# Performance work log

Hardware: AMD Instinct MI355X
Metric: run time of the kernel (lower is better)

Reference implementation:

```python
import jax, jax.numpy as jnp
import numpy as np

ALPHA = 1.702
LIMIT = 7.0


def setup_inputs() -> dict:
    key = jax.random.key(0)
    ks = jax.random.split(key, 7)
    B, S, H, D, E, TOPK = 2, 2048, 2048, 2048, 8, 4
    T = B * S
    hidden_states = jax.random.normal(ks[0], (B, S, H), dtype=jnp.float32)
    gate_up_proj = jax.random.normal(ks[1], (E, H, 2 * D), dtype=jnp.float32) * 0.02
    gate_up_proj_bias = jax.random.normal(ks[2], (E, 2 * D), dtype=jnp.float32) * 0.02
    down_proj = jax.random.normal(ks[3], (E, D, H), dtype=jnp.float32) * 0.02
    down_proj_bias = jax.random.normal(ks[4], (E, H), dtype=jnp.float32) * 0.02
    rw = jax.random.uniform(ks[5], (T, E), dtype=jnp.float32)
    routing_weights = rw / jnp.sum(rw, axis=-1, keepdims=True)
    router_indices = jax.random.randint(ks[6], (T, TOPK), 0, E, dtype=jnp.int64)
    return {
        "hidden_states": hidden_states,
        "gate_up_proj": gate_up_proj,
        "gate_up_proj_bias": gate_up_proj_bias,
        "down_proj": down_proj,
        "down_proj_bias": down_proj_bias,
        "routing_weights": routing_weights,
        "router_indices": router_indices,
    }


def geglu(gate_up):
    # interleaved layout: gate = [..., 0::2], up = [..., 1::2]
    gate = gate_up[..., 0::2]
    up = gate_up[..., 1::2]
    gate = jnp.minimum(gate, LIMIT)
    up = jnp.clip(up, -LIMIT, LIMIT)
    glu = gate * jax.nn.sigmoid(gate * ALPHA)
    return (up + 1.0) * glu


def reference(hidden_states, gate_up_proj, gate_up_proj_bias, down_proj,
              down_proj_bias, routing_weights, router_indices):
    B, S, H = hidden_states.shape
    x = hidden_states.reshape(-1, H)  # [T, H]
    # per-expert batched GEMM: [E, T, 2D]
    gate_up = jnp.einsum('th,ehd->etd', x, gate_up_proj) + gate_up_proj_bias[:, None, :]
    act = geglu(gate_up)  # [E, T, D]
    out = jnp.einsum('etd,edh->eth', act, down_proj) + down_proj_bias[:, None, :]
    # weight by router probs and sum over experts
    out = out * routing_weights.T[:, :, None]  # [E, T, H]
    out = jnp.sum(out, axis=0)
    return out.reshape(B, S, H)
```

## Files before the change

### kernel.cpp

```cpp
#include <hip/hip_runtime.h>
#include <hip/hip_bf16.h>

#define ALPHA 1.702f
#define GLIMIT 7.0f

typedef __attribute__((ext_vector_type(4))) float f32x4;
typedef __attribute__((ext_vector_type(8))) __bf16 bf16x8;
typedef __attribute__((ext_vector_type(8))) short short8;

typedef __attribute__((address_space(3))) unsigned int as3_uint;
typedef const __attribute__((address_space(1))) unsigned int as1_uint;

__device__ __forceinline__ void async_copy16(void* lds, const void* g) {
    __builtin_amdgcn_global_load_lds((as1_uint*)g, (as3_uint*)lds, 16, 0, 0);
}

__device__ __forceinline__ short f2bf(float f) {
    unsigned u = __float_as_uint(f);
    unsigned r = (u + 0x7fffu + ((u >> 16) & 1u)) >> 16;
    return (short)r;
}

__global__ void cvt_bf16_kernel(const float* __restrict__ src,
                                short* __restrict__ dst, int n4) {
    int i = blockIdx.x * blockDim.x + threadIdx.x;
    if (i < n4) {
        float4 v = reinterpret_cast<const float4*>(src)[i];
        short4 o;
        o.x = f2bf(v.x); o.y = f2bf(v.y); o.z = f2bf(v.z); o.w = f2bf(v.w);
        reinterpret_cast<short4*>(dst)[i] = o;
    }
}

__global__ void transpose_cvt(const float* __restrict__ src,
                              short* __restrict__ dst, int R, int C) {
    __shared__ float t[64][65];
    const int z  = blockIdx.z;
    const int c0 = blockIdx.x * 64;
    const int r0 = blockIdx.y * 64;
    const float* s = src + (size_t)z * R * C;
    short* d = dst + (size_t)z * R * C;
    const int tid = threadIdx.x;
#pragma unroll
    for (int i = 0; i < 16; ++i) {
        int idx = i * 256 + tid;
        int r = idx >> 6, c = idx & 63;
        t[r][c] = s[(size_t)(r0 + r) * C + c0 + c];
    }
    __syncthreads();
#pragma unroll
    for (int i = 0; i < 16; ++i) {
        int idx = i * 256 + tid;
        int r = idx >> 6, c = idx & 63;
        d[(size_t)(c0 + r) * R + r0 + c] = f2bf(t[c][r]);
    }
}


struct Gemm1PSrc {
    const short* A; const short* B;
    __device__ __forceinline__ const short* operator()(int t, int h) const {
        int e = t >> 5;
        size_t ko = (size_t)(t & 31) << 6;
        if (h & 2) return B + ((size_t)e << 23) + ((size_t)(h & 1) << 18) + ko;
        return A + ((size_t)(h & 1) << 18) + ko;
    }
};

struct Gemm2Src {
    const short* act; const short* wdt; size_t aoff, boff; int kh;
    __device__ __forceinline__ const short* operator()(int t, int h) const {
        int g = (kh << 7) + t;
        int e = g >> 5;
        size_t ko = (size_t)(g & 31) << 6;
        if (h & 2) return wdt + ((size_t)e << 22) + boff + ((size_t)(h & 1) << 18) + ko;
        return act + ((size_t)e << 23) + aoff + ((size_t)(h & 1) << 18) + ko;
    }
};

#define PH_BAR()  __builtin_amdgcn_s_barrier()
#define PH_LGKM() do { asm volatile("s_waitcnt lgkmcnt(0)" ::: "memory"); \
                       __builtin_amdgcn_sched_barrier(0); } while (0)
#define VMW(n)    asm volatile("s_waitcnt vmcnt(" #n ")" ::: "memory")

template <int NT, int SEG, typename Src, typename Epi>
__device__ __forceinline__ void gemm_8phase(const Src& src, char* smem,
                                            f32x4 (&acc)[8][4], const Epi& epi) {
    const int tid  = threadIdx.x;
    const int lane = tid & 63;
    const int wid  = tid >> 6;
    const int wr   = wid >> 2;
    const int wcol = wid & 3;
    const int lhi  = lane >> 4;
    const int llo  = lane & 15;

    auto stage = [&](int buf, int h, const short* g) {
        char* dst = smem + buf * 65536 + h * 16384;
        {
            int c = tid, r = c >> 3, s = (c & 7) ^ (r & 7);
            async_copy16(dst + c * 16, g + (size_t)r * 2048 + s * 8);
        }
        {
            int c = tid + 512, r = c >> 3, s = (c & 7) ^ (r & 7);
            async_copy16(dst + c * 16, g + (size_t)r * 2048 + s * 8);
        }
    };
    auto ldfrag = [&](int buf, int h, int row, int slot) {
        return *(const bf16x8*)(smem + buf * 65536 + h * 16384 + row * 128 +
                                ((slot ^ (row & 7)) << 4));
    };

    stage(0, 0, src(0, 0)); stage(0, 2, src(0, 2));
    stage(0, 3, src(0, 3)); stage(0, 1, src(0, 1));
    stage(1, 0, src(1, 0)); stage(1, 2, src(1, 2)); stage(1, 3, src(1, 3));
    VMW(8);
    PH_BAR();

    bf16x8 a[4][2], b[4][2];
#pragma unroll
    for (int n = 0; n < 2; ++n) {
        int row = wcol * 32 + n * 16 + llo;
        b[n][0] = ldfrag(0, 2, row, lhi);
        b[n][1] = ldfrag(0, 2, row, 4 + lhi);
    }

    for (int t = 0; t < NT; ++t) {
        const int cur = t & 1, nxt = cur ^ 1;
#pragma unroll
        for (int m = 0; m < 4; ++m) {
            int row = wr * 64 + m * 16 + llo;
            a[m][0] = ldfrag(cur, 0, row, lhi);
            a[m][1] = ldfrag(cur, 0, row, 4 + lhi);
        }
        if (t + 1 < NT) stage(nxt, 1, src(t + 1, 1));
        PH_BAR(); PH_LGKM();
        __builtin_amdgcn_s_setprio(1);
#pragma unroll
        for (int m = 0; m < 4; ++m)
#pragma unroll
            for (int n = 0; n < 2; ++n)
#pragma unroll
                for (int ks = 0; ks < 2; ++ks)
                    acc[m][n] = __builtin_amdgcn_mfma_f32_16x16x32_bf16(
                        a[m][ks], b[n][ks], acc[m][n], 0, 0, 0);
        __builtin_amdgcn_s_setprio(0);
        PH_BAR();
#pragma unroll
        for (int n = 0; n < 2; ++n) {
            int row = wcol * 32 + n * 16 + llo;
            b[2 + n][0] = ldfrag(cur, 3, row, lhi);
            b[2 + n][1] = ldfrag(cur, 3, row, 4 + lhi);
        }
        if (t + 2 < NT) { stage(cur, 0, src(t + 2, 0)); VMW(10); }
        else if (t + 1 < NT) { VMW(8); }
        else { VMW(0); }
        PH_BAR(); PH_LGKM();
        __builtin_amdgcn_s_setprio(1);
#pragma unroll
        for (int m = 0; m < 4; ++m)
#pragma unroll
            for (int n = 2; n < 4; ++n)
#pragma unroll
                for (int ks = 0; ks < 2; ++ks)
                    acc[m][n] = __builtin_amdgcn_mfma_f32_16x16x32_bf16(
                        a[m][ks], b[n][ks], acc[m][n], 0, 0, 0);
        __builtin_amdgcn_s_setprio(0);
        PH_BAR();
#pragma unroll
        for (int m = 0; m < 4; ++m) {
            int row = wr * 64 + m * 16 + llo;
            a[m][0] = ldfrag(cur, 1, row, lhi);
            a[m][1] = ldfrag(cur, 1, row, 4 + lhi);
        }
        if (t + 2 < NT) stage(cur, 2, src(t + 2, 2));
        PH_BAR(); PH_LGKM();
        __builtin_amdgcn_s_setprio(1);
#pragma unroll
        for (int m = 0; m < 4; ++m)
#pragma unroll
            for (int n = 0; n < 2; ++n)
#pragma unroll
                for (int ks = 0; ks < 2; ++ks)
                    acc[4 + m][n] = __builtin_amdgcn_mfma_f32_16x16x32_bf16(
                        a[m][ks], b[n][ks], acc[4 + m][n], 0, 0, 0);
        __builtin_amdgcn_s_setprio(0);
        PH_BAR();
        if (t + 2 < NT) { stage(cur, 3, src(t + 2, 3)); VMW(8); }
        else if (t + 1 < NT) { VMW(2); }
        else { VMW(0); }
        PH_BAR(); PH_LGKM();
        __builtin_amdgcn_s_setprio(1);
        if (t + 1 < NT) {
#pragma unroll
            for (int n = 0; n < 2; ++n) {
                int row = wcol * 32 + n * 16 + llo;
                b[n][0] = ldfrag(nxt, 2, row, lhi);
                b[n][1] = ldfrag(nxt, 2, row, 4 + lhi);
            }
        }
#pragma unroll
        for (int m = 0; m < 4; ++m)
#pragma unroll
            for (int n = 2; n < 4; ++n)
#pragma unroll
                for (int ks = 0; ks < 2; ++ks)
                    acc[4 + m][n] = __builtin_amdgcn_mfma_f32_16x16x32_bf16(
                        a[m][ks], b[n][ks], acc[4 + m][n], 0, 0, 0);
        __builtin_amdgcn_s_setprio(0);
        PH_BAR();
        if (((t + 1) & (SEG - 1)) == 0) {
            epi(t / SEG, acc);
            if (t + 1 < NT) {
                VMW(8);
#pragma unroll
                for (int m = 0; m < 8; ++m)
#pragma unroll
                    for (int n = 0; n < 4; ++n)
                        acc[m][n] = (f32x4){0.f, 0.f, 0.f, 0.f};
            }
        }
    }
}

__global__ __launch_bounds__(512, 2) void gemm1_8ph(
    const short* __restrict__ xb, const short* __restrict__ wgut,
    const float* __restrict__ bias, const float* __restrict__ rwp,
    short* __restrict__ act) {
    __shared__ __align__(16) char smem[131072];
    __shared__ float rws2[2048];
    __shared__ float bias2[2048];
    const int bid = blockIdx.x;
    const int xcd = bid & 7, j = bid >> 3;
    const int n0 = (((xcd << 1) + (j >> 4)) << 8);
    const int m0 = ((j & 15) << 8);
    const int tid  = threadIdx.x;
    const int lane = tid & 63;
    const int wid  = tid >> 6;
    const int wr = wid >> 2, wcol = wid & 3;
    const int lhi = lane >> 4, llo = lane & 15;

    ((float4*)rws2)[tid] = ((const float4*)(rwp + (size_t)m0 * 8))[tid];
    {
        int idx = tid << 2;
        int ei = idx >> 8, c = idx & 255;
        ((float4*)bias2)[tid] =
            *(const float4*)(bias + (size_t)ei * 4096 + n0 + c);
    }

    f32x4 acc[8][4];
#pragma unroll
    for (int m = 0; m < 8; ++m)
#pragma unroll
        for (int n = 0; n < 4; ++n) acc[m][n] = (f32x4){0.f, 0.f, 0.f, 0.f};

    Gemm1PSrc src{ xb + (size_t)m0 * 2048, wgut + (size_t)n0 * 2048 };
    const int par = lane & 1;

    auto epi = [&](int e, f32x4 (&ac)[8][4]) {
        short* acte = act + ((size_t)e << 23);
#pragma unroll
        for (int n = 0; n < 4; ++n) {
            int clocal = (n >> 1) * 128 + wcol * 32 + (n & 1) * 16 + llo;
            float bv = bias2[(e << 8) + clocal];
            int dcol = (n0 + clocal) >> 1;
#pragma unroll
            for (int m = 0; m < 8; ++m) {
                int rowb = (m >> 2) * 128 + wr * 64 + (m & 3) * 16 + (lhi << 2);
                float v[4], o[4];
#pragma unroll
                for (int q = 0; q < 4; ++q) v[q] = ac[m][n][q] + bv;
#pragma unroll
                for (int q = 0; q < 4; ++q) o[q] = __shfl_xor(v[q], 1);
#pragma unroll
                for (int jj = 0; jj < 2; ++jj) {
                    int q = (par << 1) + jj;
                    float g = par ? o[q] : v[q];
                    float u = par ? v[q] : o[q];
                    g = fminf(g, GLIMIT);
                    u = fmaxf(fminf(u, GLIMIT), -GLIMIT);
                    float glu = g / (1.f + __expf(-ALPHA * g));
                    int row = rowb + q;
                    float aa = (u + 1.f) * glu * rws2[row * 8 + e];
                    acte[(size_t)(m0 + row) * 2048 + dcol] = f2bf(aa);
                }
            }
        }
    };
    gemm_8phase<256, 32>(src, smem, acc, epi);
}

__global__ __launch_bounds__(512, 2) void gemm2_8ph(
    const short* __restrict__ act, const short* __restrict__ wdt,
    float* __restrict__ out, float* __restrict__ part) {
    __shared__ __align__(16) char smem[131072];
    const int kh = blockIdx.z;
    int flat = blockIdx.x + (blockIdx.y << 3);
    int swz = (flat & 7) * 16 + (flat >> 3);
    const int n0 = (swz & 7) * 256;
    const int m0 = (swz >> 3) * 256;
    const int tid  = threadIdx.x;
    const int lane = tid & 63;
    const int wid  = tid >> 6;
    const int wr = wid >> 2, wcol = wid & 3;

    f32x4 acc[8][4];
#pragma unroll
    for (int m = 0; m < 8; ++m)
#pragma unroll
        for (int n = 0; n < 4; ++n) acc[m][n] = (f32x4){0.f, 0.f, 0.f, 0.f};

    Gemm2Src src{ act, wdt, (size_t)m0 * 2048, (size_t)n0 * 2048, kh };
    float* dst = (kh == 0) ? out : part;

    auto epi = [&](int, f32x4 (&ac)[8][4]) {
#pragma unroll
        for (int m = 0; m < 8; ++m) {
            int row = m0 + (m >> 2) * 128 + wr * 64 + (m & 3) * 16 + ((lane >> 4) << 2);
#pragma unroll
            for (int n = 0; n < 4; ++n) {
                int col = n0 + (n >> 1) * 128 + wcol * 32 + (n & 1) * 16 + (lane & 15);
#pragma unroll
                for (int q = 0; q < 4; ++q)
                    dst[(size_t)(row + q) * 2048 + col] = ac[m][n][q];
            }
        }
    };
    gemm_8phase<128, 128>(src, smem, acc, epi);
}

__global__ __launch_bounds__(256) void reduce_bias(
    const float* __restrict__ p1, const float* __restrict__ rw,
    const float* __restrict__ bd, float* __restrict__ out) {
    const int t = blockIdx.x;
    const int tid = threadIdx.x;
    float rwv[8];
#pragma unroll
    for (int e = 0; e < 8; ++e) rwv[e] = rw[(size_t)t * 8 + e];
    size_t base = (size_t)t * 2048;
#pragma unroll
    for (int i = 0; i < 2; ++i) {
        int h = (tid + i * 256) * 4;
        float4 o = *(const float4*)(out + base + h);
        float4 p = *(const float4*)(p1 + base + h);
        o.x += p.x; o.y += p.y; o.z += p.z; o.w += p.w;
#pragma unroll
        for (int e = 0; e < 8; ++e) {
            float4 bb = *(const float4*)(bd + e * 2048 + h);
            o.x += rwv[e] * bb.x; o.y += rwv[e] * bb.y;
            o.z += rwv[e] * bb.z; o.w += rwv[e] * bb.w;
        }
        *(float4*)(out + base + h) = o;
    }
}

extern "C" void kernel_launch(void* const* d_in, const int* in_sizes, int n_in,
                              void* d_out, int out_size, void* d_ws, size_t ws_size,
                              hipStream_t stream) {
    const float* x   = (const float*)d_in[0];
    const float* wgu = (const float*)d_in[1];
    const float* bgu = (const float*)d_in[2];
    const float* wd  = (const float*)d_in[3];
    const float* bd  = (const float*)d_in[4];
    const float* rw  = (const float*)d_in[5];
    float* out = (float*)d_out;

    char* ws = (char*)d_ws;
    short* xb   = (short*)(ws);
    short* wgut = (short*)(ws + 16777216);
    float* p1   = (float*)(ws + 16777216);
    short* wdt  = (short*)(ws + 150994944);
    short* actb = (short*)(ws + 218103808);

    cvt_bf16_kernel<<<8192, 256, 0, stream>>>(x, xb, 2097152);
    transpose_cvt<<<dim3(64, 32, 8), 256, 0, stream>>>(wgu, wgut, 2048, 4096);
    transpose_cvt<<<dim3(32, 32, 8), 256, 0, stream>>>(wd, wdt, 2048, 2048);
    gemm1_8ph<<<256, 512, 0, stream>>>(xb, wgut, bgu, rw, actb);
    gemm2_8ph<<<dim3(8, 16, 2), 512, 0, stream>>>(actb, wdt, out, p1);
    reduce_bias<<<4096, 256, 0, stream>>>(p1, rw, bd, out);
}
```

Before: 1.093 ms.

## Permute gate/up weight columns and stage GEGLU epilogue through LDS for vector stores

The transposed gate_up weights are permuted within each 256-column tile so gate and up columns land in separate accumulator fragments. This removes the shuffle-based pairing in the epilogue and computes each output once per lane. Activation results are written into swizzled LDS slots and then stored to global memory as 16-byte vectors instead of scattered 2-byte stores. The cost is extra barriers in the epilogue and reuse of the pipeline's shared-memory buffers, which depends on removing a vmem wait and may race with in-flight prefetches.

```diff
diff --git a/kernel.cpp b/kernel.cpp
--- a/kernel.cpp
+++ b/kernel.cpp
@@ -33,7 +33,7 @@
 }
 
 __global__ void transpose_cvt(const float* __restrict__ src,
-                              short* __restrict__ dst, int R, int C) {
+                              short* __restrict__ dst, int R, int C, int perm) {
     __shared__ float t[64][65];
     const int z  = blockIdx.z;
     const int c0 = blockIdx.x * 64;
@@ -52,7 +52,10 @@
     for (int i = 0; i < 16; ++i) {
         int idx = i * 256 + tid;
         int r = idx >> 6, c = idx & 63;
-        d[(size_t)(c0 + r) * R + r0 + c] = f2bf(t[c][r]);
+        int rr = c0 + r;
+        int rloc = rr & 255;
+        int rp = perm ? ((rr & ~255) | ((rloc & 1) << 7) | (rloc >> 1)) : rr;
+        d[(size_t)rp * R + r0 + c] = f2bf(t[c][r]);
     }
 }
 
@@ -211,7 +214,6 @@
         if (((t + 1) & (SEG - 1)) == 0) {
             epi(t / SEG, acc);
             if (t + 1 < NT) {
-                VMW(8);
 #pragma unroll
                 for (int m = 0; m < 8; ++m)
 #pragma unroll
@@ -254,37 +256,57 @@
         for (int n = 0; n < 4; ++n) acc[m][n] = (f32x4){0.f, 0.f, 0.f, 0.f};
 
     Gemm1PSrc src{ xb + (size_t)m0 * 2048, wgut + (size_t)n0 * 2048 };
-    const int par = lane & 1;
+    const int a0 = n0 >> 1;
 
     auto epi = [&](int e, f32x4 (&ac)[8][4]) {
         short* acte = act + ((size_t)e << 23);
-#pragma unroll
-        for (int n = 0; n < 4; ++n) {
-            int clocal = (n >> 1) * 128 + wcol * 32 + (n & 1) * 16 + llo;
-            float bv = bias2[(e << 8) + clocal];
-            int dcol = (n0 + clocal) >> 1;
-#pragma unroll
-            for (int m = 0; m < 8; ++m) {
+        float bg[2], bu[2];
+#pragma unroll
+        for (int n = 0; n < 2; ++n) {
+            int acol = wcol * 32 + n * 16 + llo;
+            bg[n] = bias2[(e << 8) + 2 * acol];
+            bu[n] = bias2[(e << 8) + 2 * acol + 1];
+        }
+        PH_LGKM();
+        PH_BAR();
+#pragma unroll
+        for (int c = 0; c < 4; ++c) {
+            char* slot = smem + ((c & 1) ? 32768 : 81920);
+#pragma unroll
+            for (int mb = 0; mb < 2; ++mb) {
+                int m = 2 * c + mb;
                 int rowb = (m >> 2) * 128 + wr * 64 + (m & 3) * 16 + (lhi << 2);
-                float v[4], o[4];
-#pragma unroll
-                for (int q = 0; q < 4; ++q) v[q] = ac[m][n][q] + bv;
-#pragma unroll
-                for (int q = 0; q < 4; ++q) o[q] = __shfl_xor(v[q], 1);
-#pragma unroll
-                for (int jj = 0; jj < 2; ++jj) {
-                    int q = (par << 1) + jj;
-                    float g = par ? o[q] : v[q];
-                    float u = par ? v[q] : o[q];
-                    g = fminf(g, GLIMIT);
-                    u = fmaxf(fminf(u, GLIMIT), -GLIMIT);
-                    float glu = g / (1.f + __expf(-ALPHA * g));
-                    int row = rowb + q;
-                    float aa = (u + 1.f) * glu * rws2[row * 8 + e];
-                    acte[(size_t)(m0 + row) * 2048 + dcol] = f2bf(aa);
+#pragma unroll
+                for (int n = 0; n < 2; ++n) {
+                    int acol = wcol * 32 + n * 16 + llo;
+#pragma unroll
+                    for (int q = 0; q < 4; ++q) {
+                        float g = ac[m][n][q] + bg[n];
+                        float u = ac[m][n + 2][q] + bu[n];
+                        g = fminf(g, GLIMIT);
+                        u = fmaxf(fminf(u, GLIMIT), -GLIMIT);
+                        float glu = g / (1.f + __expf(-ALPHA * g));
+                        float aa = (u + 1.f) * glu * rws2[(rowb + q) * 8 + e];
+                        int lrow = wr * 32 + mb * 16 + (lhi << 2) + q;
+                        *(short*)(slot + lrow * 256 +
+                                  (((acol << 1) ^ ((lrow & 15) << 4)))) = f2bf(aa);
+                    }
                 }
             }
-        }
+            PH_LGKM();
+            PH_BAR();
+#pragma unroll
+            for (int i = 0; i < 2; ++i) {
+                int idx = i * 512 + tid;
+                int lrow = idx >> 4, g16 = idx & 15;
+                int grow = ((c >> 1) << 7) + ((lrow >> 5) << 6) +
+                           (((c & 1) * 2 + ((lrow >> 4) & 1)) << 4) + (lrow & 15);
+                short8 vv = *(const short8*)(slot + lrow * 256 +
+                                             ((g16 ^ (lrow & 15)) << 4));
+                *(short8*)(acte + (size_t)(m0 + grow) * 2048 + a0 + g16 * 8) = vv;
+            }
+        }
+        PH_BAR();
     };
     gemm_8phase<256, 32>(src, smem, acc, epi);
 }
@@ -372,8 +394,8 @@
     short* actb = (short*)(ws + 218103808);
 
     cvt_bf16_kernel<<<8192, 256, 0, stream>>>(x, xb, 2097152);
-    transpose_cvt<<<dim3(64, 32, 8), 256, 0, stream>>>(wgu, wgut, 2048, 4096);
-    transpose_cvt<<<dim3(32, 32, 8), 256, 0, stream>>>(wd, wdt, 2048, 2048);
+    transpose_cvt<<<dim3(64, 32, 8), 256, 0, stream>>>(wgu, wgut, 2048, 4096, 1);
+    transpose_cvt<<<dim3(32, 32, 8), 256, 0, stream>>>(wd, wdt, 2048, 2048, 0);
     gemm1_8ph<<<256, 512, 0, stream>>>(xb, wgut, bgu, rw, actb);
     gemm2_8ph<<<dim3(8, 16, 2), 512, 0, stream>>>(actb, wdt, out, p1);
     reduce_bias<<<4096, 256, 0, stream>>>(p1, rw, bd, out);
```

Measured after the change: 932.9 us. 1.17x faster.
